# Performance work log

Measured on AMD Instinct MI355X. Metric: run time of the kernel, lower is better.

Reference implementation:

```python
import jax, jax.numpy as jnp
import numpy as np

N_NODES = 100000
HIDDEN = 128
N_LAYERS = 3
N_EDGES = 600000


def setup_inputs() -> dict:
    key = jax.random.key(0)
    k_e, k_emb, k_w = jax.random.split(key, 3)
    edge_index = jax.random.randint(k_e, (2, N_EDGES), 0, N_NODES, dtype=jnp.int64 if jax.config.read('jax_enable_x64') else jnp.int32)
    embedding = jax.random.normal(k_emb, (N_NODES, HIDDEN), dtype=jnp.float32)
    Ws = jax.random.normal(k_w, (N_LAYERS, HIDDEN, HIDDEN), dtype=jnp.float32) * (1.0 / np.sqrt(HIDDEN))
    bs = jnp.zeros((N_LAYERS, HIDDEN), dtype=jnp.float32)
    return {"edge_index": edge_index, "embedding": embedding, "Ws": Ws, "bs": bs}


def _gcn_forward(embedding, Ws, bs, edge_index):
    N = embedding.shape[0]
    # PyG GCNConv default: add self-loops, symmetric deg^{-1/2} normalization
    loop = jnp.arange(N, dtype=edge_index.dtype)
    src = jnp.concatenate([edge_index[0], loop])  # [E+N]
    dst = jnp.concatenate([edge_index[1], loop])
    deg = jax.ops.segment_sum(jnp.ones_like(dst, dtype=embedding.dtype), dst, num_segments=N)
    dinv = jnp.where(deg > 0, jax.lax.rsqrt(jnp.where(deg > 0, deg, 1.0)), 0.0)
    norm = dinv[src] * dinv[dst]  # [E+N]

    x = embedding
    for l in range(Ws.shape[0]):
        h = x @ Ws[l]                              # [N, d] linear transform
        msg = h[src] * norm[:, None]               # gather + scale
        x = jax.ops.segment_sum(msg, dst, num_segments=N) + bs[l]  # scatter-add
        x = jax.nn.relu(x)
        # dropout is identity in eval mode
    return x


def reference(edge_index, embedding, Ws, bs):
    return _gcn_forward(embedding, Ws, bs, edge_index)
```

## Files before the change

kernel.cpp:

```cpp
#include <hip/hip_runtime.h>
#include <hip/hip_bf16.h>


#define HID 128

typedef __attribute__((ext_vector_type(8))) short short8;
typedef __attribute__((ext_vector_type(4))) float floatx4;

#define WLDS 136


__global__ void k_init_cnt(int* cnt, int n) {
    int i = blockIdx.x * blockDim.x + threadIdx.x;
    if (i < n) cnt[i] = 1;
}

__global__ void k_count_edges(const int* __restrict__ ei, int* cnt, int E) {
    int e = blockIdx.x * blockDim.x + threadIdx.x;
    if (e < E) atomicAdd(&cnt[ei[E + e]], 1);
}

__global__ void k_scanA(const int* __restrict__ cnt, int* csum, int n) {
    __shared__ int sd[256];
    int t = threadIdx.x;
    int base = blockIdx.x * 1024 + t * 4;
    int s = 0;
#pragma unroll
    for (int j = 0; j < 4; j++) { int i = base + j; if (i < n) s += cnt[i]; }
    sd[t] = s; __syncthreads();
    for (int off = 128; off > 0; off >>= 1) {
        if (t < off) sd[t] += sd[t + off];
        __syncthreads();
    }
    if (t == 0) csum[blockIdx.x] = sd[0];
}

__global__ void k_scanB(int* csum, int* offsets, int nchunk, int n) {
    __shared__ int sd[256];
    int t = threadIdx.x;
    int v = (t < nchunk) ? csum[t] : 0;
    sd[t] = v; __syncthreads();
    for (int off = 1; off < 256; off <<= 1) {
        int u = (t >= off) ? sd[t - off] : 0;
        __syncthreads();
        sd[t] += u;
        __syncthreads();
    }
    if (t < nchunk) csum[t] = sd[t] - v;
    if (t == 0) offsets[n] = sd[255];
}

__global__ void k_scanC(const int* __restrict__ cnt, const int* __restrict__ csum,
                        int* offsets, int* cursor, float* dinv,
                        int* adj_src, float* adj_norm, int n) {
    __shared__ int sd[256];
    int t = threadIdx.x;
    int base = blockIdx.x * 1024 + t * 4;
    int c[4]; int s = 0;
#pragma unroll
    for (int j = 0; j < 4; j++) {
        c[j] = (base + j < n) ? cnt[base + j] : 0;
        s += c[j];
    }
    sd[t] = s; __syncthreads();
    for (int off = 1; off < 256; off <<= 1) {
        int v = (t >= off) ? sd[t - off] : 0;
        __syncthreads();
        sd[t] += v;
        __syncthreads();
    }
    int run = sd[t] - s + csum[blockIdx.x];
#pragma unroll
    for (int j = 0; j < 4; j++) {
        int i = base + j;
        if (i < n) {
            offsets[i] = run;
            float di = rsqrtf((float)c[j]);
            dinv[i] = di;
            cursor[i] = run + 1;
            adj_src[run] = i;
            adj_norm[run] = di * di;
        }
        run += c[j];
    }
}

__global__ void k_fill_edges(const int* __restrict__ ei, int* cursor,
                             const float* __restrict__ dinv,
                             int* adj_src, float* adj_norm, int E) {
    int e = blockIdx.x * blockDim.x + threadIdx.x;
    if (e >= E) return;
    int s = ei[e];
    int d = ei[E + e];
    int pos = atomicAdd(&cursor[d], 1);
    adj_src[pos] = s;
    adj_norm[pos] = dinv[s] * dinv[d];
}

__global__ void k_packW(const float* __restrict__ Ws, ushort* Whp, ushort* Wlp,
                        int nlayers) {
    int idx = blockIdx.x * blockDim.x + threadIdx.x;
    if (idx >= nlayers * HID * HID) return;
    int l = idx >> 14;
    int n = (idx >> 7) & 127;
    int k = idx & 127;
    float w = Ws[(size_t)l * HID * HID + k * HID + n];
    __hip_bfloat16 hi = __float2bfloat16(w);
    float lo = w - __bfloat162float(hi);
    __hip_bfloat16 lo16 = __float2bfloat16(lo);
    Whp[idx] = *(ushort*)&hi;
    Wlp[idx] = *(ushort*)&lo16;
}


__global__ __launch_bounds__(256) void k_agg(const float* __restrict__ x,
                                             const int* __restrict__ offsets,
                                             const int* __restrict__ adj_src,
                                             const float* __restrict__ adj_norm,
                                             ushort* __restrict__ yh,
                                             ushort* __restrict__ yl, int n) {
    int gid = blockIdx.x * blockDim.x + threadIdx.x;
    int lane = gid & 63;
    int q    = lane >> 4;
    int ql   = lane & 15;
    int f4   = (q & 1) * 16 + ql;
    int epar = q >> 1;
    int nwaves = (gridDim.x * blockDim.x) >> 6;

    for (int node = gid >> 6; node < n; node += nwaves) {
        int beg = offsets[node];
        int end = offsets[node + 1];

        float4 acc = {0.f, 0.f, 0.f, 0.f};

        int e0 = beg + epar;
        int c0 = e0 < end ? e0 : end - 1;
        int s0 = adj_src[c0];
        float w0 = e0 < end ? adj_norm[c0] : 0.f;

        int e1 = beg + 2 + epar;
        int c1 = e1 < end ? e1 : end - 1;
        int s1 = adj_src[c1];
        float w1 = e1 < end ? adj_norm[c1] : 0.f;

        float4 v0 = ((const float4*)(x + (size_t)s0 * HID))[f4];

        for (int e = beg + 2; e < end; e += 2) {
            int e2 = e + 2 + epar;
            int c2 = e2 < end ? e2 : end - 1;
            int s2 = adj_src[c2];
            float w2 = e2 < end ? adj_norm[c2] : 0.f;

            float4 v1 = ((const float4*)(x + (size_t)s1 * HID))[f4];

            acc.x += w0 * v0.x;
            acc.y += w0 * v0.y;
            acc.z += w0 * v0.z;
            acc.w += w0 * v0.w;

            v0 = v1; w0 = w1;
            s1 = s2; w1 = w2;
        }
        acc.x += w0 * v0.x;
        acc.y += w0 * v0.y;
        acc.z += w0 * v0.z;
        acc.w += w0 * v0.w;

        acc.x += __shfl_xor(acc.x, 32);
        acc.y += __shfl_xor(acc.y, 32);
        acc.z += __shfl_xor(acc.z, 32);
        acc.w += __shfl_xor(acc.w, 32);
        if (lane < 32) {
            float a[4] = {acc.x, acc.y, acc.z, acc.w};
            ushort4 h, l;
            ushort* hp = (ushort*)&h;
            ushort* lp = (ushort*)&l;
#pragma unroll
            for (int j = 0; j < 4; j++) {
                __hip_bfloat16 hi = __float2bfloat16(a[j]);
                float lo = a[j] - __bfloat162float(hi);
                __hip_bfloat16 lo16 = __float2bfloat16(lo);
                hp[j] = *(ushort*)&hi;
                lp[j] = *(ushort*)&lo16;
            }
            ((ushort4*)(yh + (size_t)node * HID))[lane] = h;
            ((ushort4*)(yl + (size_t)node * HID))[lane] = l;
        }
    }
}


__global__ __launch_bounds__(256, 2) void k_gemm_mfma(const ushort* __restrict__ yh,
                                                      const ushort* __restrict__ yl,
                                                      const ushort* __restrict__ Whp,
                                                      const ushort* __restrict__ Wlp,
                                                      const float* __restrict__ bias,
                                                      float* __restrict__ out, int n) {
    __shared__ ushort Wh_lds[HID * WLDS];
    __shared__ ushort Wl_lds[HID * WLDS];
    int t = threadIdx.x;
    int wave = t >> 6;
    int lane = t & 63;
    int m16  = lane & 15;
    int oct  = lane >> 4;

    short8 ah[2][4], al[2][4];
#pragma unroll
    for (int mt = 0; mt < 2; mt++) {
        int rowA = blockIdx.x * 128 + wave * 32 + mt * 16 + m16;
        const ushort* hb = yh + (size_t)rowA * HID + oct * 8;
        const ushort* lb = yl + (size_t)rowA * HID + oct * 8;
#pragma unroll
        for (int ks = 0; ks < 4; ks++) {
            ah[mt][ks] = *(const short8*)(hb + ks * 32);
            al[mt][ks] = *(const short8*)(lb + ks * 32);
        }
    }

    for (int idx = t; idx < HID * 16; idx += 256) {
        int r = idx >> 4, c8 = idx & 15;
        ((uint4*)(Wh_lds + r * WLDS))[c8] = ((const uint4*)(Whp + r * HID))[c8];
        ((uint4*)(Wl_lds + r * WLDS))[c8] = ((const uint4*)(Wlp + r * HID))[c8];
    }
    __syncthreads();

    floatx4 acc0[8], acc1[8];
#pragma unroll
    for (int c = 0; c < 8; c++) {
        acc0[c] = (floatx4){0.f, 0.f, 0.f, 0.f};
        acc1[c] = (floatx4){0.f, 0.f, 0.f, 0.f};
    }

#pragma unroll
    for (int ks = 0; ks < 4; ks++) {
#pragma unroll
        for (int c = 0; c < 8; c++) {
            const ushort* bp = Wh_lds + (c * 16 + m16) * WLDS + ks * 32 + oct * 8;
            const ushort* bq = Wl_lds + (c * 16 + m16) * WLDS + ks * 32 + oct * 8;
            short8 bh = *(const short8*)bp;
            short8 bl = *(const short8*)bq;
            acc0[c] = __builtin_amdgcn_mfma_f32_16x16x32_bf16(ah[0][ks], bh, acc0[c], 0, 0, 0);
            acc0[c] = __builtin_amdgcn_mfma_f32_16x16x32_bf16(ah[0][ks], bl, acc0[c], 0, 0, 0);
            acc0[c] = __builtin_amdgcn_mfma_f32_16x16x32_bf16(al[0][ks], bh, acc0[c], 0, 0, 0);
            acc1[c] = __builtin_amdgcn_mfma_f32_16x16x32_bf16(ah[1][ks], bh, acc1[c], 0, 0, 0);
            acc1[c] = __builtin_amdgcn_mfma_f32_16x16x32_bf16(ah[1][ks], bl, acc1[c], 0, 0, 0);
            acc1[c] = __builtin_amdgcn_mfma_f32_16x16x32_bf16(al[1][ks], bh, acc1[c], 0, 0, 0);
        }
    }

#pragma unroll
    for (int mt = 0; mt < 2; mt++) {
        int rowbase = blockIdx.x * 128 + wave * 32 + mt * 16 + oct * 4;
#pragma unroll
        for (int c = 0; c < 8; c++) {
            int col = c * 16 + m16;
            float b = bias[col];
            floatx4 a = mt == 0 ? acc0[c] : acc1[c];
#pragma unroll
            for (int r = 0; r < 4; r++) {
                int row = rowbase + r;
                if (row < n) {
                    float v = fmaxf(a[r] + b, 0.f);
                    out[(size_t)row * HID + col] = v;
                }
            }
        }
    }
}


extern "C" void kernel_launch(void* const* d_in, const int* in_sizes, int n_in,
                              void* d_out, int out_size, void* d_ws, size_t ws_size,
                              hipStream_t stream) {
    const int* ei = (const int*)d_in[0];
    const float* emb = (const float*)d_in[1];
    const float* Ws = (const float*)d_in[2];
    const float* bs = (const float*)d_in[3];

    const int E = in_sizes[0] / 2;
    const int N = in_sizes[1] / HID;
    const int NL = in_sizes[3] / HID;
    const int TOT = E + N;
    const int NPAD = ((N + 127) / 128) * 128;

    char* p = (char*)d_ws;
    auto carve = [&](size_t bytes) {
        char* r = p;
        p += (bytes + 255) & ~(size_t)255;
        return (void*)r;
    };
    int*    cnt      = (int*)   carve((size_t)N * 4);
    int*    offsets  = (int*)   carve((size_t)(N + 1) * 4);
    int*    cursor   = (int*)   carve((size_t)N * 4);
    float*  dinv     = (float*) carve((size_t)N * 4);
    int*    csum     = (int*)   carve(1024 * 4);
    int*    adj_src  = (int*)   carve((size_t)TOT * 4);
    float*  adj_norm = (float*) carve((size_t)TOT * 4);
    ushort* yh       = (ushort*)carve((size_t)NPAD * HID * 2);
    ushort* yl       = (ushort*)carve((size_t)NPAD * HID * 2);
    ushort* Whp      = (ushort*)carve((size_t)NL * HID * HID * 2);
    ushort* Wlp      = (ushort*)carve((size_t)NL * HID * HID * 2);
    float*  xbufA    = (float*) carve((size_t)N * HID * 4);
    float*  xbufB    = (float*) d_out;

    const int NCHUNK = (N + 1023) / 1024;

    k_init_cnt<<<(N + 255) / 256, 256, 0, stream>>>(cnt, N);
    k_count_edges<<<(E + 255) / 256, 256, 0, stream>>>(ei, cnt, E);
    k_scanA<<<NCHUNK, 256, 0, stream>>>(cnt, csum, N);
    k_scanB<<<1, 256, 0, stream>>>(csum, offsets, NCHUNK, N);
    k_scanC<<<NCHUNK, 256, 0, stream>>>(cnt, csum, offsets, cursor, dinv,
                                        adj_src, adj_norm, N);
    k_fill_edges<<<(E + 255) / 256, 256, 0, stream>>>(ei, cursor, dinv,
                                                      adj_src, adj_norm, E);
    k_packW<<<(NL * HID * HID + 255) / 256, 256, 0, stream>>>(Ws, Whp, Wlp, NL);

    const int aggBlocks = 2048;
    const int gemmBlocks = NPAD / 128;
    const float* x = emb;
    for (int l = 0; l < NL; l++) {
        float* o = (l == 1) ? xbufA : xbufB;
        k_agg<<<aggBlocks, 256, 0, stream>>>(x, offsets, adj_src, adj_norm, yh, yl, N);
        k_gemm_mfma<<<gemmBlocks, 256, 0, stream>>>(yh, yl,
                                                    Whp + (size_t)l * HID * HID,
                                                    Wlp + (size_t)l * HID * HID,
                                                    bs + (size_t)l * HID, o, N);
        x = o;
    }
}
```

Measured before the change: 430.2 us.

## Interleave CSR source/norm into int2 and deepen aggregation gather prefetch

Packs adjacency source index and normalization weight into one int2 array, so the aggregation kernel issues a single 8-byte load per edge instead of two separate loads. The gather pipeline in k_agg is deepened so two feature rows are in flight ahead of the accumulate, and the next node's CSR offsets are prefetched during the current node's work. This is meant to hide gather latency in the memory-bound aggregation. The cost is more live registers and extra clamped loads on low-degree nodes.

```diff
diff --git a/kernel.cpp b/kernel.cpp
--- a/kernel.cpp
+++ b/kernel.cpp
@@ -52,7 +52,7 @@
 
 __global__ void k_scanC(const int* __restrict__ cnt, const int* __restrict__ csum,
                         int* offsets, int* cursor, float* dinv,
-                        int* adj_src, float* adj_norm, int n) {
+                        int2* adj, int n) {
     __shared__ int sd[256];
     int t = threadIdx.x;
     int base = blockIdx.x * 1024 + t * 4;
@@ -78,8 +78,7 @@
             float di = rsqrtf((float)c[j]);
             dinv[i] = di;
             cursor[i] = run + 1;
-            adj_src[run] = i;
-            adj_norm[run] = di * di;
+            adj[run] = make_int2(i, __float_as_int(di * di));
         }
         run += c[j];
     }
@@ -87,14 +86,13 @@
 
 __global__ void k_fill_edges(const int* __restrict__ ei, int* cursor,
                              const float* __restrict__ dinv,
-                             int* adj_src, float* adj_norm, int E) {
+                             int2* adj, int E) {
     int e = blockIdx.x * blockDim.x + threadIdx.x;
     if (e >= E) return;
     int s = ei[e];
     int d = ei[E + e];
     int pos = atomicAdd(&cursor[d], 1);
-    adj_src[pos] = s;
-    adj_norm[pos] = dinv[s] * dinv[d];
+    adj[pos] = make_int2(s, __float_as_int(dinv[s] * dinv[d]));
 }
 
 __global__ void k_packW(const float* __restrict__ Ws, ushort* Whp, ushort* Wlp,
@@ -115,8 +113,7 @@
 
 __global__ __launch_bounds__(256) void k_agg(const float* __restrict__ x,
                                              const int* __restrict__ offsets,
-                                             const int* __restrict__ adj_src,
-                                             const float* __restrict__ adj_norm,
+                                             const int2* __restrict__ adj,
                                              ushort* __restrict__ yh,
                                              ushort* __restrict__ yl, int n) {
     int gid = blockIdx.x * blockDim.x + threadIdx.x;
@@ -127,44 +124,59 @@
     int epar = q >> 1;
     int nwaves = (gridDim.x * blockDim.x) >> 6;
 
-    for (int node = gid >> 6; node < n; node += nwaves) {
-        int beg = offsets[node];
-        int end = offsets[node + 1];
+    int node0 = gid >> 6;
+    int nbeg = 0, nend = 0;
+    if (node0 < n) { nbeg = offsets[node0]; nend = offsets[node0 + 1]; }
+
+    for (int node = node0; node < n; node += nwaves) {
+        int beg = nbeg;
+        int end = nend;
+        int nxt = node + nwaves;
+        if (nxt < n) { nbeg = offsets[nxt]; nend = offsets[nxt + 1]; }
 
         float4 acc = {0.f, 0.f, 0.f, 0.f};
 
         int e0 = beg + epar;
         int c0 = e0 < end ? e0 : end - 1;
-        int s0 = adj_src[c0];
-        float w0 = e0 < end ? adj_norm[c0] : 0.f;
-
-        int e1 = beg + 2 + epar;
+        int2 a0 = adj[c0];
+        int e1 = e0 + 2;
         int c1 = e1 < end ? e1 : end - 1;
-        int s1 = adj_src[c1];
-        float w1 = e1 < end ? adj_norm[c1] : 0.f;
-
-        float4 v0 = ((const float4*)(x + (size_t)s0 * HID))[f4];
-
-        for (int e = beg + 2; e < end; e += 2) {
-            int e2 = e + 2 + epar;
-            int c2 = e2 < end ? e2 : end - 1;
-            int s2 = adj_src[c2];
-            float w2 = e2 < end ? adj_norm[c2] : 0.f;
-
-            float4 v1 = ((const float4*)(x + (size_t)s1 * HID))[f4];
+        int2 a1 = adj[c1];
+        int e2 = e0 + 4;
+        int c2 = e2 < end ? e2 : end - 1;
+        int2 a2 = adj[c2];
+        float w0 = e0 < end ? __int_as_float(a0.y) : 0.f;
+        float w1 = e1 < end ? __int_as_float(a1.y) : 0.f;
+        float w2 = e2 < end ? __int_as_float(a2.y) : 0.f;
+        float4 v0 = ((const float4*)(x + (size_t)a0.x * HID))[f4];
+        float4 v1 = ((const float4*)(x + (size_t)a1.x * HID))[f4];
+        int s2 = a2.x;
+
+        for (int e = beg + 4; e < end; e += 2) {
+            int e3 = e + 2 + epar;
+            int c3 = e3 < end ? e3 : end - 1;
+            int2 a3 = adj[c3];
+            float w3 = e3 < end ? __int_as_float(a3.y) : 0.f;
+
+            float4 v2 = ((const float4*)(x + (size_t)s2 * HID))[f4];
 
             acc.x += w0 * v0.x;
             acc.y += w0 * v0.y;
             acc.z += w0 * v0.z;
             acc.w += w0 * v0.w;
 
-            v0 = v1; w0 = w1;
-            s1 = s2; w1 = w2;
+            v0 = v1; v1 = v2;
+            w0 = w1; w1 = w2; w2 = w3;
+            s2 = a3.x;
         }
         acc.x += w0 * v0.x;
         acc.y += w0 * v0.y;
         acc.z += w0 * v0.z;
         acc.w += w0 * v0.w;
+        acc.x += w1 * v1.x;
+        acc.y += w1 * v1.y;
+        acc.z += w1 * v1.z;
+        acc.w += w1 * v1.w;
 
         acc.x += __shfl_xor(acc.x, 32);
         acc.y += __shfl_xor(acc.y, 32);
@@ -294,8 +306,7 @@
     int*    cursor   = (int*)   carve((size_t)N * 4);
     float*  dinv     = (float*) carve((size_t)N * 4);
     int*    csum     = (int*)   carve(1024 * 4);
-    int*    adj_src  = (int*)   carve((size_t)TOT * 4);
-    float*  adj_norm = (float*) carve((size_t)TOT * 4);
+    int2*   adj      = (int2*)  carve((size_t)TOT * 8);
     ushort* yh       = (ushort*)carve((size_t)NPAD * HID * 2);
     ushort* yl       = (ushort*)carve((size_t)NPAD * HID * 2);
     ushort* Whp      = (ushort*)carve((size_t)NL * HID * HID * 2);
@@ -310,9 +321,9 @@
     k_scanA<<<NCHUNK, 256, 0, stream>>>(cnt, csum, N);
     k_scanB<<<1, 256, 0, stream>>>(csum, offsets, NCHUNK, N);
     k_scanC<<<NCHUNK, 256, 0, stream>>>(cnt, csum, offsets, cursor, dinv,
-                                        adj_src, adj_norm, N);
+                                        adj, N);
     k_fill_edges<<<(E + 255) / 256, 256, 0, stream>>>(ei, cursor, dinv,
-                                                      adj_src, adj_norm, E);
+                                                      adj, E);
     k_packW<<<(NL * HID * HID + 255) / 256, 256, 0, stream>>>(Ws, Whp, Wlp, NL);
 
     const int aggBlocks = 2048;
@@ -320,7 +331,7 @@
     const float* x = emb;
     for (int l = 0; l < NL; l++) {
         float* o = (l == 1) ? xbufA : xbufB;
-        k_agg<<<aggBlocks, 256, 0, stream>>>(x, offsets, adj_src, adj_norm, yh, yl, N);
+        k_agg<<<aggBlocks, 256, 0, stream>>>(x, offsets, adj, yh, yl, N);
         k_gemm_mfma<<<gemmBlocks, 256, 0, stream>>>(yh, yl,
                                                     Whp + (size_t)l * HID * HID,
                                                     Wlp + (size_t)l * HID * HID,
```

After: 435.0 us. Within noise of the previous version (+1.1%).
